# Optimization experiments

Hardware: AMD Instinct MI355X
Metric: run time of the kernel (lower is better)

Reference implementation:

```python
import jax, jax.numpy as jnp
import numpy as np

DIM = 256
HEAD_DIM = 32
HEADS = DIM // HEAD_DIM
SCALE = HEAD_DIM ** -0.5


def setup_inputs() -> dict:
    key = jax.random.key(0)
    ks = jax.random.split(key, 5)
    B, C, H, W = 2, DIM, 48, 48
    x = jax.random.normal(ks[0], (B, C, H, W), jnp.float32)
    # qkv 1x1 conv weight [3C, C] (no bias, qkv_bias=False)
    w_qkv = jax.random.normal(ks[1], (3 * C, C), jnp.float32) * (C ** -0.5)
    # depthwise 3x3 conv (groups=C): weight [C, 1, 3, 3] + bias [C]
    w_lepe = jax.random.normal(ks[2], (C, 1, 3, 3), jnp.float32) * (1.0 / 3.0)
    b_lepe = jax.random.normal(ks[3], (C,), jnp.float32) * 0.01
    # proj 1x1 conv weight [C, C] + bias [C]
    w_proj = jax.random.normal(ks[4], (C, C), jnp.float32) * (C ** -0.5)
    b_proj = jnp.zeros((C,), jnp.float32)
    return {"x": x, "w_qkv": w_qkv, "w_lepe": w_lepe, "b_lepe": b_lepe,
            "w_proj": w_proj, "b_proj": b_proj}


def reference(x, w_qkv, w_lepe, b_lepe, w_proj, b_proj):
    B, C, H, W = x.shape
    N = H * W
    h, d = HEADS, HEAD_DIM
    # qkv 1x1 conv -> [B, 3C, H, W], reshape to [B, h, 3d, N], chunk on dim 2
    qkv = jnp.einsum('oc,bchw->bohw', w_qkv, x).reshape(B, h, 3 * d, N)
    q, k, v = jnp.split(qkv, 3, axis=2)  # each [B, h, d, N]
    # lepe: depthwise 3x3 conv on v reshaped back to [B, C, H, W]
    v4 = v.reshape(B, C, H, W)
    lepe = jax.lax.conv_general_dilated(
        v4, w_lepe, window_strides=(1, 1), padding='SAME',
        dimension_numbers=('NCHW', 'OIHW', 'NCHW'),
        feature_group_count=C) + b_lepe[None, :, None, None]
    # attn = k^T @ q * scale, softmax over the KEY dim (dim=-2)
    attn = jax.nn.softmax(jnp.einsum('bhdk,bhdq->bhkq', k, q) * SCALE, axis=-2)
    # out = v @ attn -> [B, h, d, N] -> [B, C, H, W]
    out = jnp.einsum('bhdk,bhkq->bhdq', v, attn).reshape(B, C, H, W)
    out = out + lepe
    # proj 1x1 conv + bias (dropouts are identity at p=0)
    out = jnp.einsum('oc,bchw->bohw', w_proj, out) + b_proj[None, :, None, None]
    return out
```

## Files before the change

### kernel.cpp

```cpp
#include <hip/hip_runtime.h>
#include <hip/hip_bf16.h>

typedef __bf16 bf16;
typedef __bf16 bf16x8 __attribute__((ext_vector_type(8)));
typedef __bf16 bf16x4 __attribute__((ext_vector_type(4)));
typedef float  f32x4  __attribute__((ext_vector_type(4)));
typedef float  f32x2  __attribute__((ext_vector_type(2)));

#define NB    2
#define CCH   256
#define NPIX  2304
#define WIMG  48
#define SLOG2E 0.25503487f
#define NSPLIT 2
#define KHALF  1152
#define TK     128
#define NITER  9

__global__ __launch_bounds__(256) void qkv_gemm(const float* __restrict__ x,
                                                const float* __restrict__ w,
                                                bf16* __restrict__ Qt,
                                                bf16* __restrict__ Kt,
                                                bf16* __restrict__ Vb) {
    __shared__ __align__(16) bf16 xT[64][40];
    const int tid  = threadIdx.x;
    const int lane = tid & 63;
    const int wv   = tid >> 6;
    const int wn   = wv & 1, wo = wv >> 1;
    const int l15  = lane & 15, l4 = lane >> 4;
    const int g0 = blockIdx.x * 64;
    const int b  = g0 / NPIX;
    const int n0 = g0 % NPIX;
    const int o0 = blockIdx.y * 64;
    const float* xb = x + (size_t)b * CCH * NPIX;

    f32x4 acc[2][2] = {};

    for (int kc = 0; kc < 8; ++kc) {
        const int c0 = kc * 32;
        for (int r = 0; r < 8; ++r) {
            int idx = r * 256 + tid;
            int c = idx >> 6, n = idx & 63;
            xT[n][c] = (bf16)xb[(size_t)(c0 + c) * NPIX + n0 + n];
        }
        __syncthreads();
        bf16x8 afr[2], bfr[2];
        for (int at = 0; at < 2; ++at) {
            const float* wp = w + (size_t)(o0 + wo * 32 + at * 16 + l15) * CCH + c0 + l4 * 8;
            f32x4 w0 = *(const f32x4*)wp;
            f32x4 w1 = *(const f32x4*)(wp + 4);
            bf16x8 a;
            for (int i = 0; i < 4; ++i) { a[i] = (bf16)w0[i]; a[i + 4] = (bf16)w1[i]; }
            afr[at] = a;
        }
        for (int bt = 0; bt < 2; ++bt)
            bfr[bt] = *(const bf16x8*)&xT[wn * 32 + bt * 16 + l15][l4 * 8];
        for (int at = 0; at < 2; ++at)
            for (int bt = 0; bt < 2; ++bt)
                acc[at][bt] = __builtin_amdgcn_mfma_f32_16x16x32_bf16(afr[at], bfr[bt],
                                                                     acc[at][bt], 0, 0, 0);
        __syncthreads();
    }

    for (int at = 0; at < 2; ++at) {
        const int otile = o0 + wo * 32 + at * 16;
        const int h    = otile / 96;
        const int role = (otile % 96) / 32;
        const int ddb  = (otile % 32) + l4 * 4;
        const int bh   = b * 8 + h;
        for (int bt = 0; bt < 2; ++bt) {
            const int n = n0 + wn * 32 + bt * 16 + l15;
            if (role == 2) {
                for (int r = 0; r < 4; ++r)
                    Vb[(size_t)(bh * 32 + ddb + r) * NPIX + n] = (bf16)acc[at][bt][r];
            } else if (role == 1) {
                bf16x4 pk;
                for (int r = 0; r < 4; ++r) pk[r] = (bf16)(acc[at][bt][r] * SLOG2E);
                *(bf16x4*)&Kt[((size_t)bh * NPIX + n) * 32 + ddb] = pk;
            } else {
                bf16x4 pk;
                for (int r = 0; r < 4; ++r) pk[r] = (bf16)acc[at][bt][r];
                *(bf16x4*)&Qt[((size_t)bh * NPIX + n) * 32 + ddb] = pk;
            }
        }
    }
}

__global__ __launch_bounds__(256, 4) void attn_kernel(const bf16* __restrict__ Qt,
                                                      const bf16* __restrict__ Kt,
                                                      const bf16* __restrict__ Vb,
                                                      float* __restrict__ Opart,
                                                      float* __restrict__ MLpart) {
    __shared__ __align__(16) bf16 Ktile[128][40];
    __shared__ __align__(16) bf16 Vtile[32][136];
    __shared__ __align__(16) bf16 Ptile[64][136];
    const int tid  = threadIdx.x;
    const int lane = tid & 63;
    const int wv   = tid >> 6;
    const int l15  = lane & 15, l4 = lane >> 4;
    const int bh    = blockIdx.y;
    const int split = blockIdx.z;
    const int q0 = blockIdx.x * 64;
    const int q  = q0 + wv * 16 + l15;

    const bf16* Kbh = Kt + (size_t)bh * NPIX * 32 + (size_t)split * KHALF * 32;
    const bf16* Vbh = Vb + (size_t)bh * 32 * NPIX + split * KHALF;

    bf16x8 qf = *(const bf16x8*)&Qt[((size_t)bh * NPIX + q) * 32 + l4 * 8];

    const int krow = tid >> 1, kcol = (tid & 1) * 16;
    const int vd   = tid >> 3, vc   = (tid & 7) * 16;
    const bf16* ksrc = Kbh + (size_t)krow * 32 + kcol;
    const bf16* vsrc = Vbh + (size_t)vd * NPIX + vc;

    bf16x8 ka, kb, va, vb_;
    ka  = *(const bf16x8*)(ksrc);
    kb  = *(const bf16x8*)(ksrc + 8);
    va  = *(const bf16x8*)(vsrc);
    vb_ = *(const bf16x8*)(vsrc + 8);
    *(bf16x8*)&Ktile[krow][kcol]     = ka;
    *(bf16x8*)&Ktile[krow][kcol + 8] = kb;
    *(bf16x8*)&Vtile[vd][vc]         = va;
    *(bf16x8*)&Vtile[vd][vc + 8]     = vb_;
    __syncthreads();

    f32x4 O0 = {}, O1 = {};
    float m_run = -INFINITY, l_run = 0.f;
    const int qrow = wv * 16 + l15;

    for (int kt = 0; kt < NITER; ++kt) {
        if (kt + 1 < NITER) {
            const bf16* ks = ksrc + (size_t)(kt + 1) * TK * 32;
            const bf16* vs = vsrc + (kt + 1) * TK;
            ka  = *(const bf16x8*)(ks);
            kb  = *(const bf16x8*)(ks + 8);
            va  = *(const bf16x8*)(vs);
            vb_ = *(const bf16x8*)(vs + 8);
        }

        f32x4 s[8];
        for (int rt = 0; rt < 8; ++rt) {
            bf16x8 a = *(const bf16x8*)&Ktile[rt * 16 + l15][l4 * 8];
            f32x4 z = {};
            s[rt] = __builtin_amdgcn_mfma_f32_16x16x32_bf16(a, qf, z, 0, 0, 0);
        }

        float tmax = -INFINITY;
        for (int rt = 0; rt < 8; ++rt)
            for (int r = 0; r < 4; ++r) tmax = fmaxf(tmax, s[rt][r]);
        tmax = fmaxf(tmax, __shfl_xor(tmax, 16));
        tmax = fmaxf(tmax, __shfl_xor(tmax, 32));
        const float m_new = fmaxf(m_run, tmax);
        const float f = __builtin_amdgcn_exp2f(m_run - m_new);
        float psum = 0.f;
        for (int rt = 0; rt < 8; ++rt) {
            bf16x4 pk;
            for (int r = 0; r < 4; ++r) {
                float p = __builtin_amdgcn_exp2f(s[rt][r] - m_new);
                psum += p;
                pk[r] = (bf16)p;
            }
            *(bf16x4*)&Ptile[qrow][rt * 16 + l4 * 4] = pk;
        }
        psum += __shfl_xor(psum, 16);
        psum += __shfl_xor(psum, 32);
        l_run = l_run * f + psum;
        m_run = m_new;
        for (int i = 0; i < 4; ++i) { O0[i] *= f; O1[i] *= f; }

        for (int ks = 0; ks < 4; ++ks) {
            bf16x8 pb = *(const bf16x8*)&Ptile[qrow][ks * 32 + l4 * 8];
            bf16x8 v0 = *(const bf16x8*)&Vtile[l15][ks * 32 + l4 * 8];
            bf16x8 v1 = *(const bf16x8*)&Vtile[16 + l15][ks * 32 + l4 * 8];
            O0 = __builtin_amdgcn_mfma_f32_16x16x32_bf16(v0, pb, O0, 0, 0, 0);
            O1 = __builtin_amdgcn_mfma_f32_16x16x32_bf16(v1, pb, O1, 0, 0, 0);
        }
        __syncthreads();
        if (kt + 1 < NITER) {
            *(bf16x8*)&Ktile[krow][kcol]     = ka;
            *(bf16x8*)&Ktile[krow][kcol + 8] = kb;
            *(bf16x8*)&Vtile[vd][vc]         = va;
            *(bf16x8*)&Vtile[vd][vc + 8]     = vb_;
        }
        __syncthreads();
    }

    f32x4* Op4 = (f32x4*)(Opart + ((size_t)(split * 16 + bh) * NPIX + q) * 32);
    Op4[l4]     = O0;
    Op4[4 + l4] = O1;
    if (l4 == 0) {
        f32x2 ml; ml[0] = m_run; ml[1] = l_run;
        *(f32x2*)&MLpart[((size_t)(split * 16 + bh) * NPIX + q) * 2] = ml;
    }
}

__global__ __launch_bounds__(256) void combine_kernel(const float* __restrict__ Opart,
                                                      const float* __restrict__ MLpart,
                                                      bf16* __restrict__ aout) {
    const int tid = threadIdx.x;
    const int qq = tid & 63, dg = tid >> 6;
    const int bh = blockIdx.y;
    const int q  = blockIdx.x * 64 + qq;
    f32x2 ml0 = *(const f32x2*)&MLpart[((size_t)bh * NPIX + q) * 2];
    f32x2 ml1 = *(const f32x2*)&MLpart[((size_t)(16 + bh) * NPIX + q) * 2];
    const float m  = fmaxf(ml0[0], ml1[0]);
    const float w0 = __builtin_amdgcn_exp2f(ml0[0] - m);
    const float w1 = __builtin_amdgcn_exp2f(ml1[0] - m);
    const float inv = 1.f / (w0 * ml0[1] + w1 * ml1[1]);
    const f32x4* p0 = (const f32x4*)&Opart[((size_t)bh * NPIX + q) * 32 + dg * 8];
    const f32x4* p1 = (const f32x4*)&Opart[((size_t)(16 + bh) * NPIX + q) * 32 + dg * 8];
    f32x4 a0 = p0[0], b0 = p0[1], a1 = p1[0], b1 = p1[1];
    for (int j = 0; j < 4; ++j) {
        a0[j] = (w0 * a0[j] + w1 * a1[j]) * inv;
        b0[j] = (w0 * b0[j] + w1 * b1[j]) * inv;
    }
    for (int j = 0; j < 4; ++j) {
        aout[(size_t)(bh * 32 + dg * 8 + j)     * NPIX + q] = (bf16)a0[j];
        aout[(size_t)(bh * 32 + dg * 8 + 4 + j) * NPIX + q] = (bf16)b0[j];
    }
}

__global__ __launch_bounds__(256) void lepe_kernel(const bf16* __restrict__ Vb,
                                                   const float* __restrict__ wl,
                                                   const float* __restrict__ bl,
                                                   bf16* __restrict__ aout) {
    __shared__ float vp[WIMG * WIMG];
    const int bc = blockIdx.x;
    const int c  = bc & 255;
    const bf16* src = Vb + (size_t)bc * NPIX;
    bf16* dst = aout + (size_t)bc * NPIX;
    const int tid = threadIdx.x;
    for (int r = 0; r < 9; ++r) vp[r * 256 + tid] = (float)src[r * 256 + tid];
    __syncthreads();
    float wgt[9];
    for (int i = 0; i < 9; ++i) wgt[i] = wl[c * 9 + i];
    const float bias = bl[c];
    for (int r = 0; r < 9; ++r) {
        const int idx = r * 256 + tid;
        const int y = idx / WIMG, xx = idx % WIMG;
        float acc = bias;
        for (int dy = 0; dy < 3; ++dy) {
            const int yy = y + dy - 1;
            if (yy < 0 || yy >= WIMG) continue;
            for (int dx = 0; dx < 3; ++dx) {
                const int xc = xx + dx - 1;
                if (xc < 0 || xc >= WIMG) continue;
                acc += vp[yy * WIMG + xc] * wgt[dy * 3 + dx];
            }
        }
        dst[idx] = (bf16)((float)dst[idx] + acc);
    }
}

__global__ __launch_bounds__(256) void proj_gemm(const bf16* __restrict__ ain,
                                                 const float* __restrict__ w,
                                                 const float* __restrict__ bp,
                                                 float* __restrict__ out) {
    __shared__ __align__(16) bf16 aT[64][40];
    const int tid  = threadIdx.x;
    const int lane = tid & 63;
    const int wv   = tid >> 6;
    const int wn   = wv & 1, wo = wv >> 1;
    const int l15  = lane & 15, l4 = lane >> 4;
    const int g0 = blockIdx.x * 64;
    const int b  = g0 / NPIX;
    const int n0 = g0 % NPIX;
    const int o0 = blockIdx.y * 64;
    const bf16* ab = ain + (size_t)b * CCH * NPIX;

    f32x4 acc[2][2] = {};
    for (int kc = 0; kc < 8; ++kc) {
        const int c0 = kc * 32;
        for (int r = 0; r < 8; ++r) {
            int idx = r * 256 + tid;
            int ci = idx >> 6, n = idx & 63;
            aT[n][ci] = ab[(size_t)(c0 + ci) * NPIX + n0 + n];
        }
        __syncthreads();
        bf16x8 afr[2], bfr[2];
        for (int at = 0; at < 2; ++at) {
            const float* wp = w + (size_t)(o0 + wo * 32 + at * 16 + l15) * CCH + c0 + l4 * 8;
            f32x4 w0 = *(const f32x4*)wp;
            f32x4 w1 = *(const f32x4*)(wp + 4);
            bf16x8 a;
            for (int i = 0; i < 4; ++i) { a[i] = (bf16)w0[i]; a[i + 4] = (bf16)w1[i]; }
            afr[at] = a;
        }
        for (int bt = 0; bt < 2; ++bt)
            bfr[bt] = *(const bf16x8*)&aT[wn * 32 + bt * 16 + l15][l4 * 8];
        for (int at = 0; at < 2; ++at)
            for (int bt = 0; bt < 2; ++bt)
                acc[at][bt] = __builtin_amdgcn_mfma_f32_16x16x32_bf16(afr[at], bfr[bt],
                                                                     acc[at][bt], 0, 0, 0);
        __syncthreads();
    }
    for (int at = 0; at < 2; ++at)
        for (int bt = 0; bt < 2; ++bt) {
            const int n = n0 + wn * 32 + bt * 16 + l15;
            for (int r = 0; r < 4; ++r) {
                const int o = o0 + wo * 32 + at * 16 + l4 * 4 + r;
                out[(size_t)(b * 256 + o) * NPIX + n] = acc[at][bt][r] + bp[o];
            }
        }
}

extern "C" void kernel_launch(void* const* d_in, const int* in_sizes, int n_in,
                              void* d_out, int out_size, void* d_ws, size_t ws_size,
                              hipStream_t stream) {
    const float* x      = (const float*)d_in[0];
    const float* w_qkv  = (const float*)d_in[1];
    const float* w_lepe = (const float*)d_in[2];
    const float* b_lepe = (const float*)d_in[3];
    const float* w_proj = (const float*)d_in[4];
    const float* b_proj = (const float*)d_in[5];
    float* out = (float*)d_out;

    bf16* Qt   = (bf16*)d_ws;
    bf16* Kt   = Qt + 1179648;
    bf16* Vb   = Kt + 1179648;
    bf16* aout = Vb + 1179648;
    float* Opart  = (float*)((char*)d_ws + 9437184);
    float* MLpart = Opart + 2359296;

    qkv_gemm     <<<dim3(72, 12),   256, 0, stream>>>(x, w_qkv, Qt, Kt, Vb);
    attn_kernel  <<<dim3(36, 16, 2), 256, 0, stream>>>(Qt, Kt, Vb, Opart, MLpart);
    combine_kernel<<<dim3(36, 16),  256, 0, stream>>>(Opart, MLpart, aout);
    lepe_kernel  <<<dim3(512),      256, 0, stream>>>(Vb, w_lepe, b_lepe, aout);
    proj_gemm    <<<dim3(72, 4),    256, 0, stream>>>(aout, w_proj, b_proj, out);
}
```

Before: 161.1 us.

## Read K/V directly from global in attention and fuse combine with LePE

The attention kernel stops staging K and V tiles in shared memory and reads MFMA operands straight from global memory, which removes two barriers per iteration and the register prefetch. The split-combine and depthwise LePE kernels are merged into one epilogue kernel that merges the partial outputs, applies the 3x3 conv by reading V directly from global, and writes aout once. This drops one launch and one read-modify-write of aout. In exchange, the attention loop relies on L1/L2 caching for K/V that all four waves re-read, and the epilogue uses scalar, less coalesced Opart reads and redundant neighbour loads.

```diff
diff --git a/kernel.cpp b/kernel.cpp
--- a/kernel.cpp
+++ b/kernel.cpp
@@ -91,8 +91,6 @@
                                                       const bf16* __restrict__ Vb,
                                                       float* __restrict__ Opart,
                                                       float* __restrict__ MLpart) {
-    __shared__ __align__(16) bf16 Ktile[128][40];
-    __shared__ __align__(16) bf16 Vtile[32][136];
     __shared__ __align__(16) bf16 Ptile[64][136];
     const int tid  = threadIdx.x;
     const int lane = tid & 63;
@@ -108,39 +106,16 @@
 
     bf16x8 qf = *(const bf16x8*)&Qt[((size_t)bh * NPIX + q) * 32 + l4 * 8];
 
-    const int krow = tid >> 1, kcol = (tid & 1) * 16;
-    const int vd   = tid >> 3, vc   = (tid & 7) * 16;
-    const bf16* ksrc = Kbh + (size_t)krow * 32 + kcol;
-    const bf16* vsrc = Vbh + (size_t)vd * NPIX + vc;
-
-    bf16x8 ka, kb, va, vb_;
-    ka  = *(const bf16x8*)(ksrc);
-    kb  = *(const bf16x8*)(ksrc + 8);
-    va  = *(const bf16x8*)(vsrc);
-    vb_ = *(const bf16x8*)(vsrc + 8);
-    *(bf16x8*)&Ktile[krow][kcol]     = ka;
-    *(bf16x8*)&Ktile[krow][kcol + 8] = kb;
-    *(bf16x8*)&Vtile[vd][vc]         = va;
-    *(bf16x8*)&Vtile[vd][vc + 8]     = vb_;
-    __syncthreads();
-
     f32x4 O0 = {}, O1 = {};
     float m_run = -INFINITY, l_run = 0.f;
     const int qrow = wv * 16 + l15;
 
     for (int kt = 0; kt < NITER; ++kt) {
-        if (kt + 1 < NITER) {
-            const bf16* ks = ksrc + (size_t)(kt + 1) * TK * 32;
-            const bf16* vs = vsrc + (kt + 1) * TK;
-            ka  = *(const bf16x8*)(ks);
-            kb  = *(const bf16x8*)(ks + 8);
-            va  = *(const bf16x8*)(vs);
-            vb_ = *(const bf16x8*)(vs + 8);
-        }
+        const int k0 = kt * TK;
 
         f32x4 s[8];
         for (int rt = 0; rt < 8; ++rt) {
-            bf16x8 a = *(const bf16x8*)&Ktile[rt * 16 + l15][l4 * 8];
+            bf16x8 a = *(const bf16x8*)&Kbh[(size_t)(k0 + rt * 16 + l15) * 32 + l4 * 8];
             f32x4 z = {};
             s[rt] = __builtin_amdgcn_mfma_f32_16x16x32_bf16(a, qf, z, 0, 0, 0);
         }
@@ -170,19 +145,11 @@
 
         for (int ks = 0; ks < 4; ++ks) {
             bf16x8 pb = *(const bf16x8*)&Ptile[qrow][ks * 32 + l4 * 8];
-            bf16x8 v0 = *(const bf16x8*)&Vtile[l15][ks * 32 + l4 * 8];
-            bf16x8 v1 = *(const bf16x8*)&Vtile[16 + l15][ks * 32 + l4 * 8];
+            bf16x8 v0 = *(const bf16x8*)&Vbh[(size_t)l15 * NPIX + k0 + ks * 32 + l4 * 8];
+            bf16x8 v1 = *(const bf16x8*)&Vbh[(size_t)(16 + l15) * NPIX + k0 + ks * 32 + l4 * 8];
             O0 = __builtin_amdgcn_mfma_f32_16x16x32_bf16(v0, pb, O0, 0, 0, 0);
             O1 = __builtin_amdgcn_mfma_f32_16x16x32_bf16(v1, pb, O1, 0, 0, 0);
         }
-        __syncthreads();
-        if (kt + 1 < NITER) {
-            *(bf16x8*)&Ktile[krow][kcol]     = ka;
-            *(bf16x8*)&Ktile[krow][kcol + 8] = kb;
-            *(bf16x8*)&Vtile[vd][vc]         = va;
-            *(bf16x8*)&Vtile[vd][vc + 8]     = vb_;
-        }
-        __syncthreads();
     }
 
     f32x4* Op4 = (f32x4*)(Opart + ((size_t)(split * 16 + bh) * NPIX + q) * 32);
@@ -194,61 +161,47 @@
     }
 }
 
-__global__ __launch_bounds__(256) void combine_kernel(const float* __restrict__ Opart,
-                                                      const float* __restrict__ MLpart,
-                                                      bf16* __restrict__ aout) {
+__global__ __launch_bounds__(256) void epilogue_kernel(const float* __restrict__ Opart,
+                                                       const float* __restrict__ MLpart,
+                                                       const bf16* __restrict__ Vb,
+                                                       const float* __restrict__ wl,
+                                                       const float* __restrict__ bl,
+                                                       bf16* __restrict__ aout) {
     const int tid = threadIdx.x;
-    const int qq = tid & 63, dg = tid >> 6;
-    const int bh = blockIdx.y;
-    const int q  = blockIdx.x * 64 + qq;
-    f32x2 ml0 = *(const f32x2*)&MLpart[((size_t)bh * NPIX + q) * 2];
-    f32x2 ml1 = *(const f32x2*)&MLpart[((size_t)(16 + bh) * NPIX + q) * 2];
-    const float m  = fmaxf(ml0[0], ml1[0]);
-    const float w0 = __builtin_amdgcn_exp2f(ml0[0] - m);
-    const float w1 = __builtin_amdgcn_exp2f(ml1[0] - m);
-    const float inv = 1.f / (w0 * ml0[1] + w1 * ml1[1]);
-    const f32x4* p0 = (const f32x4*)&Opart[((size_t)bh * NPIX + q) * 32 + dg * 8];
-    const f32x4* p1 = (const f32x4*)&Opart[((size_t)(16 + bh) * NPIX + q) * 32 + dg * 8];
-    f32x4 a0 = p0[0], b0 = p0[1], a1 = p1[0], b1 = p1[1];
-    for (int j = 0; j < 4; ++j) {
-        a0[j] = (w0 * a0[j] + w1 * a1[j]) * inv;
-        b0[j] = (w0 * b0[j] + w1 * b1[j]) * inv;
-    }
-    for (int j = 0; j < 4; ++j) {
-        aout[(size_t)(bh * 32 + dg * 8 + j)     * NPIX + q] = (bf16)a0[j];
-        aout[(size_t)(bh * 32 + dg * 8 + 4 + j) * NPIX + q] = (bf16)b0[j];
-    }
-}
-
-__global__ __launch_bounds__(256) void lepe_kernel(const bf16* __restrict__ Vb,
-                                                   const float* __restrict__ wl,
-                                                   const float* __restrict__ bl,
-                                                   bf16* __restrict__ aout) {
-    __shared__ float vp[WIMG * WIMG];
-    const int bc = blockIdx.x;
-    const int c  = bc & 255;
-    const bf16* src = Vb + (size_t)bc * NPIX;
-    bf16* dst = aout + (size_t)bc * NPIX;
-    const int tid = threadIdx.x;
-    for (int r = 0; r < 9; ++r) vp[r * 256 + tid] = (float)src[r * 256 + tid];
-    __syncthreads();
+    const int bh  = blockIdx.y;
+    const int q0  = blockIdx.x * 64;
+    const int d   = tid >> 3;
+    const int n8  = (tid & 7) * 8;
+    const int c   = bh * 32 + d;
+    const int ch  = c & 255;
+    const float bias = bl[ch];
     float wgt[9];
-    for (int i = 0; i < 9; ++i) wgt[i] = wl[c * 9 + i];
-    const float bias = bl[c];
-    for (int r = 0; r < 9; ++r) {
-        const int idx = r * 256 + tid;
-        const int y = idx / WIMG, xx = idx % WIMG;
+    for (int i = 0; i < 9; ++i) wgt[i] = wl[ch * 9 + i];
+    const bf16* vrow = Vb + (size_t)c * NPIX;
+
+    for (int j = 0; j < 8; ++j) {
+        const int q = q0 + n8 + j;
+        f32x2 ml0 = *(const f32x2*)&MLpart[((size_t)bh * NPIX + q) * 2];
+        f32x2 ml1 = *(const f32x2*)&MLpart[((size_t)(16 + bh) * NPIX + q) * 2];
+        const float m  = fmaxf(ml0[0], ml1[0]);
+        const float w0 = __builtin_amdgcn_exp2f(ml0[0] - m);
+        const float w1 = __builtin_amdgcn_exp2f(ml1[0] - m);
+        const float inv = 1.f / (w0 * ml0[1] + w1 * ml1[1]);
+        const float o0 = Opart[((size_t)bh * NPIX + q) * 32 + d];
+        const float o1 = Opart[((size_t)(16 + bh) * NPIX + q) * 32 + d];
+        float val = (w0 * o0 + w1 * o1) * inv;
+        const int y = q / WIMG, xx = q % WIMG;
         float acc = bias;
-        for (int dy = 0; dy < 3; ++dy) {
-            const int yy = y + dy - 1;
+        for (int dy = -1; dy <= 1; ++dy) {
+            const int yy = y + dy;
             if (yy < 0 || yy >= WIMG) continue;
-            for (int dx = 0; dx < 3; ++dx) {
-                const int xc = xx + dx - 1;
+            for (int dx = -1; dx <= 1; ++dx) {
+                const int xc = xx + dx;
                 if (xc < 0 || xc >= WIMG) continue;
-                acc += vp[yy * WIMG + xc] * wgt[dy * 3 + dx];
-            }
-        }
-        dst[idx] = (bf16)((float)dst[idx] + acc);
+                acc += (float)vrow[yy * WIMG + xc] * wgt[(dy + 1) * 3 + dx + 1];
+            }
+        }
+        aout[(size_t)c * NPIX + q] = (bf16)(val + acc);
     }
 }
 
@@ -322,9 +275,8 @@
     float* Opart  = (float*)((char*)d_ws + 9437184);
     float* MLpart = Opart + 2359296;
 
-    qkv_gemm     <<<dim3(72, 12),   256, 0, stream>>>(x, w_qkv, Qt, Kt, Vb);
-    attn_kernel  <<<dim3(36, 16, 2), 256, 0, stream>>>(Qt, Kt, Vb, Opart, MLpart);
-    combine_kernel<<<dim3(36, 16),  256, 0, stream>>>(Opart, MLpart, aout);
-    lepe_kernel  <<<dim3(512),      256, 0, stream>>>(Vb, w_lepe, b_lepe, aout);
-    proj_gemm    <<<dim3(72, 4),    256, 0, stream>>>(aout, w_proj, b_proj, out);
-}
+    qkv_gemm      <<<dim3(72, 12),    256, 0, stream>>>(x, w_qkv, Qt, Kt, Vb);
+    attn_kernel   <<<dim3(36, 16, 2), 256, 0, stream>>>(Qt, Kt, Vb, Opart, MLpart);
+    epilogue_kernel<<<dim3(36, 16),   256, 0, stream>>>(Opart, MLpart, Vb, w_lepe, b_lepe, aout);
+    proj_gemm     <<<dim3(72, 4),     256, 0, stream>>>(aout, w_proj, b_proj, out);
+}
```

After: 200.2 us. +24.3%, slower.
